# Kernel optimization log

Hardware: AMD Instinct MI355X
Metric: run time of the kernel (lower is better)

## Reference

```python
import jax, jax.numpy as jnp
import numpy as np

THRESHOLD = 0.95
SECONDARY = 0.5


def setup_inputs() -> dict:
    key = jax.random.key(0)
    quantum_states = jax.random.normal(key, (8, 2048, 64), dtype=jnp.float32)
    return {"quantum_states": quantum_states}


def reference(quantum_states):
    # quantum_states: (B, N, D)
    B, N, D = quantum_states.shape
    # pairwise fidelity: (states @ states^T)^2 -> (B, N, N)
    dots = jnp.einsum("bnd,bmd->bnm", quantum_states, quantum_states)
    fid = dots * dots
    # edge weights: 1.0 if fid >= threshold, else SECONDARY if fid >= secondary, else 0
    w = jnp.where(fid >= THRESHOLD, jnp.float32(1.0),
                  jnp.where(fid >= SECONDARY, jnp.float32(SECONDARY), jnp.float32(0.0)))
    # zero out diagonal (only i < j pairs form edges)
    eye = jnp.eye(N, dtype=bool)
    w = jnp.where(eye[None, :, :], jnp.float32(0.0), w)
    # Laplacian L = D - W
    deg = jnp.sum(w, axis=-1)  # (B, N)
    lap = -w
    idx = jnp.arange(N)
    lap = lap.at[:, idx, idx].set(deg)
    return lap
```

## Files before the change

### kernel.cpp

```cpp
#include <hip/hip_runtime.h>

typedef __attribute__((ext_vector_type(8))) __bf16 bf16x8;
typedef __attribute__((ext_vector_type(4))) __bf16 bf16x4;
typedef __attribute__((ext_vector_type(4))) float f32x4;

#define LDST 68

#define T_HI 0.97467943f
#define T_LO 0.70710678f

__device__ __forceinline__ void lds_barrier() {
    asm volatile("s_waitcnt lgkmcnt(0)" ::: "memory");
    __builtin_amdgcn_s_barrier();
    __builtin_amdgcn_sched_barrier(0);
}
__device__ __forceinline__ void full_barrier() {
    asm volatile("s_waitcnt vmcnt(0) lgkmcnt(0)" ::: "memory");
    __builtin_amdgcn_s_barrier();
    __builtin_amdgcn_sched_barrier(0);
}

__global__ __launch_bounds__(1024, 4) void lap_strip64_kernel(
    const float* __restrict__ X, float* __restrict__ out, int N)
{
    const int flat   = blockIdx.x;
    const int b      = flat & 7;
    const int strip0 = (flat >> 3) * 64;
    const int tid  = threadIdx.x;
    const int lane = tid & 63;
    const int w    = tid >> 6;
    const int t    = lane & 15;
    const int g    = lane >> 4;

    __shared__ __align__(16) unsigned short As[2][256 * LDST];
    __shared__ __align__(16) unsigned short Bs[64 * LDST];
    __shared__ float deg_part[16][64];

    const float* Xb   = X   + (size_t)b * N * 64;
    float*       outb = out + (size_t)b * N * N;

    {
        const float4* src = reinterpret_cast<const float4*>(Xb + (size_t)strip0 * 64);
        int r = tid >> 4, q = tid & 15;
        float4 v = src[tid];
        bf16x4 h = {(__bf16)v.x, (__bf16)v.y, (__bf16)v.z, (__bf16)v.w};
        *reinterpret_cast<bf16x4*>(&Bs[r * LDST + q * 4]) = h;
    }

    float4 pre[4];
    {
        const float4* src = reinterpret_cast<const float4*>(Xb);
#pragma unroll
        for (int it = 0; it < 4; ++it) pre[it] = src[tid + it * 1024];
#pragma unroll
        for (int it = 0; it < 4; ++it) {
            int idx = tid + it * 1024;
            int r = idx >> 4, q = idx & 15;
            float4 v = pre[it];
            bf16x4 h = {(__bf16)v.x, (__bf16)v.y, (__bf16)v.z, (__bf16)v.w};
            *reinterpret_cast<bf16x4*>(&As[0][r * LDST + q * 4]) = h;
        }
    }
    lds_barrier();

    bf16x8 bfrag[2][4];
#pragma unroll
    for (int ks = 0; ks < 2; ++ks)
#pragma unroll
        for (int fj = 0; fj < 4; ++fj)
            bfrag[ks][fj] = *reinterpret_cast<const bf16x8*>(
                &Bs[(16 * fj + t) * LDST + ks * 32 + g * 8]);

    float rs[4] = {0.f, 0.f, 0.f, 0.f};
    int cur = 0;
    const int nct = N >> 8;
    const int diag_ct = strip0 >> 8;

    for (int ct = 0; ct < nct; ++ct) {
        if (ct + 1 < nct) {
            const float4* src = reinterpret_cast<const float4*>(Xb + (size_t)(ct + 1) * 256 * 64);
#pragma unroll
            for (int it = 0; it < 4; ++it) pre[it] = src[tid + it * 1024];
        }

        f32x4 acc[4] = {};
#pragma unroll
        for (int ks = 0; ks < 2; ++ks) {
            const int koff = ks * 32 + g * 8;
            bf16x8 a = *reinterpret_cast<const bf16x8*>(
                &As[cur][(16 * w + t) * LDST + koff]);
#pragma unroll
            for (int fj = 0; fj < 4; ++fj)
                acc[fj] = __builtin_amdgcn_mfma_f32_16x16x32_bf16(
                    a, bfrag[ks][fj], acc[fj], 0, 0, 0);
        }

        const bool has_diag = (ct == diag_ct);
        const int ocol0 = ct * 256 + 16 * w + 4 * g;
#pragma unroll
        for (int fj = 0; fj < 4; ++fj) {
            const int orow = strip0 + 16 * fj + t;
            float wv[4];
#pragma unroll
            for (int r = 0; r < 4; ++r) {
                const float d = acc[fj][r];
                float wt = (fabsf(d) >= T_HI) ? 1.0f
                         : ((fabsf(d) >= T_LO) ? 0.5f : 0.0f);
                if (has_diag && (ocol0 + r == orow)) wt = 0.0f;
                rs[fj] += wt;
                wv[r] = -wt;
            }
            f32x4 st = {wv[0], wv[1], wv[2], wv[3]};
            *reinterpret_cast<f32x4*>(&outb[(size_t)orow * N + ocol0]) = st;
        }

        if (ct + 1 < nct) {
#pragma unroll
            for (int it = 0; it < 4; ++it) {
                int idx = tid + it * 1024;
                int r = idx >> 4, q = idx & 15;
                float4 v = pre[it];
                bf16x4 h = {(__bf16)v.x, (__bf16)v.y, (__bf16)v.z, (__bf16)v.w};
                *reinterpret_cast<bf16x4*>(&As[cur ^ 1][r * LDST + q * 4]) = h;
            }
        }
        lds_barrier();
        cur ^= 1;
    }

#pragma unroll
    for (int fj = 0; fj < 4; ++fj) {
        rs[fj] += __shfl_xor(rs[fj], 16, 64);
        rs[fj] += __shfl_xor(rs[fj], 32, 64);
    }
    if (g == 0) {
#pragma unroll
        for (int fj = 0; fj < 4; ++fj) deg_part[w][16 * fj + t] = rs[fj];
    }
    full_barrier();
    if (tid < 64) {
        float d = 0.f;
#pragma unroll
        for (int ww = 0; ww < 16; ++ww) d += deg_part[ww][tid];
        const int rr = strip0 + tid;
        outb[(size_t)rr * N + rr] = d;
    }
}

extern "C" void kernel_launch(void* const* d_in, const int* in_sizes, int n_in,
                              void* d_out, int out_size, void* d_ws, size_t ws_size,
                              hipStream_t stream) {
    const float* X = (const float*)d_in[0];
    float* out = (float*)d_out;

    const int B = 8;
    const int D = 64;
    const int N = in_sizes[0] / (B * D);

    dim3 grid((N / 64) * B);
    lap_strip64_kernel<<<grid, dim3(1024), 0, stream>>>(X, out, N);
}
```

Measured before the change: 29.71 us.

## Make A-tile staging wave-private to remove per-iteration block barriers

Each wave now loads, converts and double-buffers only the 16 rows of the column tile it consumes, in its own LDS region. This removes the block-wide barrier after every column tile, so waves can run independently. The cost is relying on intra-wave ordering of LDS writes and reads without explicit barriers, and a different global load pattern.

New measurement: 30.48 us. 1.03x slower.

```diff
diff --git a/kernel.cpp b/kernel.cpp
--- a/kernel.cpp
+++ b/kernel.cpp
@@ -9,18 +9,7 @@
 #define T_HI 0.97467943f
 #define T_LO 0.70710678f
 
-__device__ __forceinline__ void lds_barrier() {
-    asm volatile("s_waitcnt lgkmcnt(0)" ::: "memory");
-    __builtin_amdgcn_s_barrier();
-    __builtin_amdgcn_sched_barrier(0);
-}
-__device__ __forceinline__ void full_barrier() {
-    asm volatile("s_waitcnt vmcnt(0) lgkmcnt(0)" ::: "memory");
-    __builtin_amdgcn_s_barrier();
-    __builtin_amdgcn_sched_barrier(0);
-}
-
-__global__ __launch_bounds__(1024, 4) void lap_strip64_kernel(
+__global__ __launch_bounds__(1024, 4) void lap_nobar_kernel(
     const float* __restrict__ X, float* __restrict__ out, int N)
 {
     const int flat   = blockIdx.x;
@@ -32,8 +21,8 @@
     const int t    = lane & 15;
     const int g    = lane >> 4;
 
-    __shared__ __align__(16) unsigned short As[2][256 * LDST];
     __shared__ __align__(16) unsigned short Bs[64 * LDST];
+    __shared__ __align__(16) unsigned short Aw[16][2][16 * LDST];
     __shared__ float deg_part[16][64];
 
     const float* Xb   = X   + (size_t)b * N * 64;
@@ -46,22 +35,7 @@
         bf16x4 h = {(__bf16)v.x, (__bf16)v.y, (__bf16)v.z, (__bf16)v.w};
         *reinterpret_cast<bf16x4*>(&Bs[r * LDST + q * 4]) = h;
     }
-
-    float4 pre[4];
-    {
-        const float4* src = reinterpret_cast<const float4*>(Xb);
-#pragma unroll
-        for (int it = 0; it < 4; ++it) pre[it] = src[tid + it * 1024];
-#pragma unroll
-        for (int it = 0; it < 4; ++it) {
-            int idx = tid + it * 1024;
-            int r = idx >> 4, q = idx & 15;
-            float4 v = pre[it];
-            bf16x4 h = {(__bf16)v.x, (__bf16)v.y, (__bf16)v.z, (__bf16)v.w};
-            *reinterpret_cast<bf16x4*>(&As[0][r * LDST + q * 4]) = h;
-        }
-    }
-    lds_barrier();
+    __syncthreads();
 
     bf16x8 bfrag[2][4];
 #pragma unroll
@@ -71,24 +45,44 @@
             bfrag[ks][fj] = *reinterpret_cast<const bf16x8*>(
                 &Bs[(16 * fj + t) * LDST + ks * 32 + g * 8]);
 
+    float4 pre[4];
+
+#define LOADP(ct_)                                                              \
+    {                                                                           \
+        const float4* src_ = reinterpret_cast<const float4*>(                   \
+            Xb + (size_t)(256 * (ct_) + 16 * w) * 64);                          \
+        _Pragma("unroll")                                                       \
+        for (int j = 0; j < 4; ++j) pre[j] = src_[j * 64 + lane];               \
+    }
+
+#define STAGEP(buf_)                                                            \
+    {                                                                           \
+        _Pragma("unroll")                                                       \
+        for (int j = 0; j < 4; ++j) {                                           \
+            int idx_ = j * 64 + lane;                                           \
+            int r_ = idx_ >> 4, q_ = idx_ & 15;                                 \
+            float4 v_ = pre[j];                                                 \
+            bf16x4 h_ = {(__bf16)v_.x, (__bf16)v_.y, (__bf16)v_.z, (__bf16)v_.w}; \
+            *reinterpret_cast<bf16x4*>(&Aw[w][buf_][r_ * LDST + q_ * 4]) = h_;  \
+        }                                                                       \
+    }
+
     float rs[4] = {0.f, 0.f, 0.f, 0.f};
-    int cur = 0;
     const int nct = N >> 8;
     const int diag_ct = strip0 >> 8;
 
+    LOADP(0);
+    STAGEP(0);
+    int cur = 0;
+
     for (int ct = 0; ct < nct; ++ct) {
-        if (ct + 1 < nct) {
-            const float4* src = reinterpret_cast<const float4*>(Xb + (size_t)(ct + 1) * 256 * 64);
-#pragma unroll
-            for (int it = 0; it < 4; ++it) pre[it] = src[tid + it * 1024];
-        }
+        if (ct + 1 < nct) LOADP(ct + 1);
 
         f32x4 acc[4] = {};
 #pragma unroll
         for (int ks = 0; ks < 2; ++ks) {
-            const int koff = ks * 32 + g * 8;
             bf16x8 a = *reinterpret_cast<const bf16x8*>(
-                &As[cur][(16 * w + t) * LDST + koff]);
+                &Aw[w][cur][t * LDST + ks * 32 + g * 8]);
 #pragma unroll
             for (int fj = 0; fj < 4; ++fj)
                 acc[fj] = __builtin_amdgcn_mfma_f32_16x16x32_bf16(
@@ -114,19 +108,11 @@
             *reinterpret_cast<f32x4*>(&outb[(size_t)orow * N + ocol0]) = st;
         }
 
-        if (ct + 1 < nct) {
-#pragma unroll
-            for (int it = 0; it < 4; ++it) {
-                int idx = tid + it * 1024;
-                int r = idx >> 4, q = idx & 15;
-                float4 v = pre[it];
-                bf16x4 h = {(__bf16)v.x, (__bf16)v.y, (__bf16)v.z, (__bf16)v.w};
-                *reinterpret_cast<bf16x4*>(&As[cur ^ 1][r * LDST + q * 4]) = h;
-            }
-        }
-        lds_barrier();
+        if (ct + 1 < nct) STAGEP(cur ^ 1);
         cur ^= 1;
     }
+#undef LOADP
+#undef STAGEP
 
 #pragma unroll
     for (int fj = 0; fj < 4; ++fj) {
@@ -137,7 +123,7 @@
 #pragma unroll
         for (int fj = 0; fj < 4; ++fj) deg_part[w][16 * fj + t] = rs[fj];
     }
-    full_barrier();
+    __syncthreads();
     if (tid < 64) {
         float d = 0.f;
 #pragma unroll
@@ -158,5 +144,5 @@
     const int N = in_sizes[0] / (B * D);
 
     dim3 grid((N / 64) * B);
-    lap_strip64_kernel<<<grid, dim3(1024), 0, stream>>>(X, out, N);
+    lap_nobar_kernel<<<grid, dim3(1024), 0, stream>>>(X, out, N);
 }
```
